# Kernel optimization log

Hardware: AMD Instinct MI355X
Metric: run time of the kernel (lower is better)

Reference implementation:

```python
import jax, jax.numpy as jnp
import numpy as np

VOCAB, EMBED, HIDDEN = 32000, 256, 512
N, L = 64, 2048

def setup_inputs() -> dict:
    key = jax.random.key(0)
    k1, k2, k3, k4 = jax.random.split(key, 4)
    X = jax.random.randint(k1, (N, L), 0, VOCAB)
    E = jax.random.normal(k2, (VOCAB, EMBED), dtype=jnp.float32) * 0.02
    W_hh = jax.random.normal(k3, (HIDDEN, HIDDEN), dtype=jnp.float32) / np.sqrt(HIDDEN)
    b_hh = jnp.zeros((HIDDEN,), dtype=jnp.float32)
    W_xh = jax.random.normal(k4, (EMBED, HIDDEN), dtype=jnp.float32) / np.sqrt(EMBED)
    b_xh = jnp.zeros((HIDDEN,), dtype=jnp.float32)
    return {"X": X, "E": E, "W_hh": W_hh, "b_hh": b_hh, "W_xh": W_xh, "b_xh": b_xh}

def reference(X, E, W_hh, b_hh, W_xh, b_xh):
    # Embed tokens: (N, L, De)
    xe = E[X]
    # Precompute input projection for all timesteps in one big GEMM: (N, L, H)
    xp = jnp.einsum('nld,dh->nlh', xe, W_xh) + b_xh
    h0 = jnp.zeros((X.shape[0], W_hh.shape[0]), dtype=E.dtype)

    def step(h, x_t):
        # h: (N, H); x_t: (N, H) already projected
        h_new = jnp.tanh(h @ W_hh + b_hh + x_t)
        return h_new, None

    # scan over time: move L to leading axis -> (L, N, H)
    h_last, _ = jax.lax.scan(step, h0, jnp.swapaxes(xp, 0, 1))
    return h_last
```

## Files before the change

kernel.cpp:

```cpp
#include <hip/hip_runtime.h>

typedef _Float16 h8 __attribute__((ext_vector_type(8)));
typedef float f4v __attribute__((ext_vector_type(4)));
typedef unsigned int u32;
typedef unsigned long long u64;
typedef u32 u32x4 __attribute__((ext_vector_type(4)));

#define SEQ 2048
#define HID 512
#define EMB 256
#define NV 32000
#define LOSCALE 2048.0f
#define INV_LOSCALE 4.8828125e-4f

#define WS_WHI 0u
#define WS_WLO (512u * 1024u)
#define WS_HG (1024u * 1024u)
#define WS_FLAGS (WS_HG + 256u * 1024u)
#define WS_PROJ (WS_FLAGS + 4u * 1024u)
#define FLAG_STRIDE 32

__global__ void wsplit_kernel(const float* __restrict__ Whh,
                              _Float16* __restrict__ Whi,
                              _Float16* __restrict__ Wlo) {
  int gid = blockIdx.x * 256 + threadIdx.x;
  int l = gid & 63, c = gid >> 6;
  int kb = c & 15, jtg = c >> 4;
  int j = jtg * 16 + (l & 15);
  int k0 = kb * 32 + (l >> 4) * 8;
  _Float16 hi[8], lo[8];
#pragma unroll
  for (int e = 0; e < 8; ++e) {
    float v = Whh[(k0 + e) * HID + j];
    _Float16 h = (_Float16)v;
    hi[e] = h;
    lo[e] = (_Float16)((v - (float)h) * LOSCALE);
  }
  *(h8*)(Whi + (size_t)gid * 8) = *(const h8*)hi;
  *(h8*)(Wlo + (size_t)gid * 8) = *(const h8*)lo;
}

template <bool PF32>
__global__ __launch_bounds__(256) void proj_kernel(const float* __restrict__ E,
                                                   const float* __restrict__ Wxh,
                                                   const float* __restrict__ bxh,
                                                   void* __restrict__ projE) {
  __shared__ float El[32 * EMB];
  const int t = threadIdx.x;
  const int v0 = blockIdx.x * 32;
  {
    const float4* src = (const float4*)(E + (size_t)v0 * EMB);
    float4* dst = (float4*)El;
#pragma unroll
    for (int i = 0; i < 8; ++i) dst[t + i * 256] = src[t + i * 256];
  }
  __syncthreads();
  const int c0 = (t & 63) * 8;
  const int rg = t >> 6;
  float acc[8][8];
#pragma unroll
  for (int r = 0; r < 8; ++r)
#pragma unroll
    for (int c = 0; c < 8; ++c) acc[r][c] = 0.f;

#pragma unroll 4
  for (int d = 0; d < EMB; ++d) {
    float wv[8];
    *(float4*)&wv[0] = *(const float4*)&Wxh[d * HID + c0];
    *(float4*)&wv[4] = *(const float4*)&Wxh[d * HID + c0 + 4];
#pragma unroll
    for (int r = 0; r < 8; ++r) {
      float ev = El[(rg * 8 + r) * EMB + d];
#pragma unroll
      for (int c = 0; c < 8; ++c) acc[r][c] = fmaf(ev, wv[c], acc[r][c]);
    }
  }
  float bv[8];
  *(float4*)&bv[0] = *(const float4*)&bxh[c0];
  *(float4*)&bv[4] = *(const float4*)&bxh[c0 + 4];
#pragma unroll
  for (int r = 0; r < 8; ++r) {
    int row = v0 + rg * 8 + r;
    if (PF32) {
      float o[8];
#pragma unroll
      for (int c = 0; c < 8; ++c) o[c] = acc[r][c] + bv[c];
      *(float4*)((float*)projE + (size_t)row * HID + c0) = *(const float4*)&o[0];
      *(float4*)((float*)projE + (size_t)row * HID + c0 + 4) = *(const float4*)&o[4];
    } else {
      _Float16 o[8];
#pragma unroll
      for (int c = 0; c < 8; ++c) o[c] = (_Float16)(acc[r][c] + bv[c]);
      *(h8*)((_Float16*)projE + (size_t)row * HID + c0) = *(const h8*)o;
    }
  }
}

__global__ void init_kernel(float4* __restrict__ p) {
  int gid = blockIdx.x * 256 + threadIdx.x;
  if (gid < 16640) p[gid] = (float4){0.f, 0.f, 0.f, 0.f};
}

template <bool PF32>
__global__ __launch_bounds__(512, 2) void rnn_kernel(
    const int* __restrict__ X, const _Float16* __restrict__ Whi,
    const _Float16* __restrict__ Wlo, const void* __restrict__ projE,
    const float* __restrict__ bhh, u32* __restrict__ hX,
    u32* __restrict__ flags, float* __restrict__ out) {
  __shared__ u32 hs[8192];
  const int tid = threadIdx.x;
  const int w = tid >> 6, lane = tid & 63;
  const int g = lane >> 4, li = lane & 15;
  const int grp = blockIdx.x >> 2, cb = blockIdx.x & 3;
  const int nb = grp * 16;
  const int jtg = cb * 8 + w;
  const int j = jtg * 16 + li;

  h8 Wh[16], Wl[16];
  {
    const char* wb = (const char*)Whi + ((size_t)jtg * 16 * 64 + lane) * 16;
    const char* wb2 = (const char*)Wlo + ((size_t)jtg * 16 * 64 + lane) * 16;
#pragma unroll
    for (int kb = 0; kb < 16; ++kb) {
      Wh[kb] = *(const h8*)(wb + (size_t)kb * 1024);
      Wl[kb] = *(const h8*)(wb2 + (size_t)kb * 1024);
    }
#pragma unroll
    for (int kb = 0; kb < 16; ++kb) {
      f4v th = __builtin_bit_cast(f4v, Wh[kb]);
      f4v tl = __builtin_bit_cast(f4v, Wl[kb]);
      asm volatile("" : "+v"(th), "+v"(tl));
      Wh[kb] = __builtin_bit_cast(h8, th);
      Wl[kb] = __builtin_bit_cast(h8, tl);
    }
  }
  const float bias = bhh[j];
  u32* fl = flags + grp * 4 * FLAG_STRIDE;

  const int hi2 = ((jtg & 1) << 1) | (li >> 3);
  const int pub0 = (li & 1) * 4096 + (jtg >> 1) * 256 + (hi2 << 6) + g * 16 +
                   ((li & 7) >> 1);
  u32* const hgrp = hX + grp * 8192;
  const bool oddli = (li & 1) != 0;

  const int* Xr[4];
#pragma unroll
  for (int i = 0; i < 4; ++i) Xr[i] = X + (size_t)(nb + g * 4 + i) * SEQ;

  for (int t = 0; t < SEQ; ++t) {
    float pv[4];
#pragma unroll
    for (int i = 0; i < 4; ++i) {
      int tok = Xr[i][t];
      if (PF32)
        pv[i] = ((const float*)projE)[(size_t)tok * HID + j];
      else
        pv[i] = (float)((const _Float16*)projE)[(size_t)tok * HID + j];
    }

    if (t > 0 && lane < 4) {
      u32 spins = 0;
      while (__hip_atomic_load(fl + lane * FLAG_STRIDE, __ATOMIC_RELAXED,
                               __HIP_MEMORY_SCOPE_AGENT) < (u32)t) {
        if (++spins > 10000u) break;
      }
    }

    {
      const u32* src = hgrp + (t & 1) * 32768;
      u64 v[4][2];
#pragma unroll
      for (int q = 0; q < 4; ++q) {
        int idx = tid * 4 + q * 2048;
        v[q][0] = __hip_atomic_load((const u64*)(src + idx), __ATOMIC_RELAXED,
                                    __HIP_MEMORY_SCOPE_AGENT);
        v[q][1] = __hip_atomic_load((const u64*)(src + idx + 2),
                                    __ATOMIC_RELAXED, __HIP_MEMORY_SCOPE_AGENT);
      }
#pragma unroll
      for (int q = 0; q < 4; ++q) {
        u32x4 d;
        d[0] = (u32)v[q][0]; d[1] = (u32)(v[q][0] >> 32);
        d[2] = (u32)v[q][1]; d[3] = (u32)(v[q][1] >> 32);
        *(u32x4*)(hs + tid * 4 + q * 2048) = d;
      }
    }
    __syncthreads();

    f4v a1 = {0.f, 0.f, 0.f, 0.f};
    f4v c1 = {0.f, 0.f, 0.f, 0.f};
    f4v c2 = {0.f, 0.f, 0.f, 0.f};
    const u32* hb_hi = hs + lane * 4;
    const u32* hb_lo = hs + 4096 + lane * 4;
#pragma unroll
    for (int kb = 0; kb < 16; ++kb) {
      h8 ahc = *(const h8*)(hb_hi + kb * 256);
      h8 alc = *(const h8*)(hb_lo + kb * 256);
      a1 = __builtin_amdgcn_mfma_f32_16x16x32_f16(ahc, Wh[kb], a1, 0, 0, 0);
      c1 = __builtin_amdgcn_mfma_f32_16x16x32_f16(ahc, Wl[kb], c1, 0, 0, 0);
      c2 = __builtin_amdgcn_mfma_f32_16x16x32_f16(alc, Wh[kb], c2, 0, 0, 0);
    }

    u32* const hn = hgrp + ((t + 1) & 1) * 32768;
    const bool lastt = (t == SEQ - 1);
#pragma unroll
    for (int i = 0; i < 4; ++i) {
      float v = a1[i] + INV_LOSCALE * (c1[i] + c2[i]) + bias + pv[i];
      float e2 = __expf(2.0f * v);
      float th = 1.0f - 2.0f / (e2 + 1.0f);
      _Float16 hh = (_Float16)th;
      _Float16 hl = (_Float16)((th - (float)hh) * LOSCALE);
      u32 pk = (u32)__builtin_bit_cast(unsigned short, hh) |
               ((u32)__builtin_bit_cast(unsigned short, hl) << 16);
      u32 nbv = (u32)__shfl_xor((int)pk, 1, 64);
      u32 word = oddli ? ((nbv >> 16) | (pk & 0xFFFF0000u))
                       : ((pk & 0xFFFFu) | (nbv << 16));
      __hip_atomic_store(hn + pub0 + i * 4, word, __ATOMIC_RELAXED,
                         __HIP_MEMORY_SCOPE_AGENT);
      if (lastt) out[(nb + g * 4 + i) * HID + j] = th;
    }
    __syncthreads();
    if (tid == 0) {
      __hip_atomic_store(fl + cb * FLAG_STRIDE, (u32)(t + 1), __ATOMIC_RELAXED,
                         __HIP_MEMORY_SCOPE_AGENT);
    }
  }
}

extern "C" void kernel_launch(void* const* d_in, const int* in_sizes, int n_in,
                              void* d_out, int out_size, void* d_ws,
                              size_t ws_size, hipStream_t stream) {
  const int* X = (const int*)d_in[0];
  const float* E = (const float*)d_in[1];
  const float* Whh = (const float*)d_in[2];
  const float* bhh = (const float*)d_in[3];
  const float* Wxh = (const float*)d_in[4];
  const float* bxh = (const float*)d_in[5];
  float* out = (float*)d_out;

  char* ws = (char*)d_ws;
  _Float16* Whi = (_Float16*)(ws + WS_WHI);
  _Float16* Wlo = (_Float16*)(ws + WS_WLO);
  u32* hX = (u32*)(ws + WS_HG);
  u32* flags = (u32*)(ws + WS_FLAGS);
  void* projE = (void*)(ws + WS_PROJ);
  const bool pf32 = ws_size >= (size_t)WS_PROJ + (size_t)NV * HID * sizeof(float);

  wsplit_kernel<<<128, 256, 0, stream>>>(Whh, Whi, Wlo);
  init_kernel<<<65, 256, 0, stream>>>((float4*)(ws + WS_HG));
  if (pf32) {
    proj_kernel<true><<<NV / 32, 256, 0, stream>>>(E, Wxh, bxh, projE);
    rnn_kernel<true><<<16, 512, 0, stream>>>(X, Whi, Wlo, projE, bhh, hX, flags, out);
  } else {
    proj_kernel<false><<<NV / 32, 256, 0, stream>>>(E, Wxh, bxh, projE);
    rnn_kernel<false><<<16, 512, 0, stream>>>(X, Whi, Wlo, projE, bhh, hX, flags, out);
  }
}
```

Measured before the change: 6.248 ms.

## Keep own hidden slice in double-buffered LDS and split flag waits per wave pair

Each block now writes its freshly computed hidden-state slice directly into a double-buffered shared array, so it only reloads the other three blocks' slices from global memory. Each wave pair waits on the flag of only the one peer block whose slice it loads, rather than every wave waiting on all four flags. This cuts global traffic and shortens the critical-path wait in the per-timestep cross-block exchange. It doubles LDS use and relies on correct ordering between the local writes and the barrier; the spin limit is also raised.

```diff
diff --git a/kernel.cpp b/kernel.cpp
--- a/kernel.cpp
+++ b/kernel.cpp
@@ -107,7 +107,7 @@
     const _Float16* __restrict__ Wlo, const void* __restrict__ projE,
     const float* __restrict__ bhh, u32* __restrict__ hX,
     u32* __restrict__ flags, float* __restrict__ out) {
-  __shared__ u32 hs[8192];
+  __shared__ u32 hs[2][8192];
   const int tid = threadIdx.x;
   const int w = tid >> 6, lane = tid & 63;
   const int g = lane >> 4, li = lane & 15;
@@ -115,6 +115,9 @@
   const int nb = grp * 16;
   const int jtg = cb * 8 + w;
   const int j = jtg * 16 + li;
+  const int pairq = w >> 1;
+  const bool ownpair = (pairq == cb);
+  const int p = (w & 1) * 64 + lane;
 
   h8 Wh[16], Wl[16];
   {
@@ -143,6 +146,9 @@
   u32* const hgrp = hX + grp * 8192;
   const bool oddli = (li & 1) != 0;
 
+#pragma unroll
+  for (int i = 0; i < 16; ++i) hs[0][tid + i * 512] = 0u;
+
   const int* Xr[4];
 #pragma unroll
   for (int i = 0; i < 4; ++i) Xr[i] = X + (size_t)(nb + g * 4 + i) * SEQ;
@@ -158,31 +164,36 @@
         pv[i] = (float)((const _Float16*)projE)[(size_t)tok * HID + j];
     }
 
-    if (t > 0 && lane < 4) {
-      u32 spins = 0;
-      while (__hip_atomic_load(fl + lane * FLAG_STRIDE, __ATOMIC_RELAXED,
-                               __HIP_MEMORY_SCOPE_AGENT) < (u32)t) {
-        if (++spins > 10000u) break;
+    if (!ownpair) {
+      if (t > 0 && lane == 0) {
+        u32 spins = 0;
+        while (__hip_atomic_load(fl + pairq * FLAG_STRIDE, __ATOMIC_RELAXED,
+                                 __HIP_MEMORY_SCOPE_AGENT) < (u32)t) {
+          if (++spins > 50000u) break;
+        }
       }
-    }
-
-    {
+      asm volatile("" ::: "memory");
       const u32* src = hgrp + (t & 1) * 32768;
-      u64 v[4][2];
-#pragma unroll
-      for (int q = 0; q < 4; ++q) {
-        int idx = tid * 4 + q * 2048;
-        v[q][0] = __hip_atomic_load((const u64*)(src + idx), __ATOMIC_RELAXED,
-                                    __HIP_MEMORY_SCOPE_AGENT);
-        v[q][1] = __hip_atomic_load((const u64*)(src + idx + 2),
-                                    __ATOMIC_RELAXED, __HIP_MEMORY_SCOPE_AGENT);
+      const int b0 = pairq * 1024 + p * 8;
+      u64 v[2][4];
+#pragma unroll
+      for (int c = 0; c < 2; ++c) {
+        const u32* s = src + b0 + c * 4096;
+#pragma unroll
+        for (int q = 0; q < 4; ++q)
+          v[c][q] = __hip_atomic_load((const u64*)(s + q * 2),
+                                      __ATOMIC_RELAXED,
+                                      __HIP_MEMORY_SCOPE_AGENT);
       }
 #pragma unroll
-      for (int q = 0; q < 4; ++q) {
-        u32x4 d;
-        d[0] = (u32)v[q][0]; d[1] = (u32)(v[q][0] >> 32);
-        d[2] = (u32)v[q][1]; d[3] = (u32)(v[q][1] >> 32);
-        *(u32x4*)(hs + tid * 4 + q * 2048) = d;
+      for (int c = 0; c < 2; ++c) {
+        u32x4 d0, d1;
+        d0[0] = (u32)v[c][0]; d0[1] = (u32)(v[c][0] >> 32);
+        d0[2] = (u32)v[c][1]; d0[3] = (u32)(v[c][1] >> 32);
+        d1[0] = (u32)v[c][2]; d1[1] = (u32)(v[c][2] >> 32);
+        d1[2] = (u32)v[c][3]; d1[3] = (u32)(v[c][3] >> 32);
+        *(u32x4*)(&hs[t & 1][b0 + c * 4096]) = d0;
+        *(u32x4*)(&hs[t & 1][b0 + c * 4096 + 4]) = d1;
       }
     }
     __syncthreads();
@@ -190,8 +201,8 @@
     f4v a1 = {0.f, 0.f, 0.f, 0.f};
     f4v c1 = {0.f, 0.f, 0.f, 0.f};
     f4v c2 = {0.f, 0.f, 0.f, 0.f};
-    const u32* hb_hi = hs + lane * 4;
-    const u32* hb_lo = hs + 4096 + lane * 4;
+    const u32* hb_hi = &hs[t & 1][lane * 4];
+    const u32* hb_lo = hb_hi + 4096;
 #pragma unroll
     for (int kb = 0; kb < 16; ++kb) {
       h8 ahc = *(const h8*)(hb_hi + kb * 256);
@@ -202,6 +213,7 @@
     }
 
     u32* const hn = hgrp + ((t + 1) & 1) * 32768;
+    u32* const hsn = hs[(t + 1) & 1];
     const bool lastt = (t == SEQ - 1);
 #pragma unroll
     for (int i = 0; i < 4; ++i) {
@@ -217,6 +229,7 @@
                        : ((pk & 0xFFFFu) | (nbv << 16));
       __hip_atomic_store(hn + pub0 + i * 4, word, __ATOMIC_RELAXED,
                          __HIP_MEMORY_SCOPE_AGENT);
+      hsn[pub0 + i * 4] = word;
       if (lastt) out[(nb + g * 4 + i) * HID + j] = th;
     }
     __syncthreads();
```

Measured after the change: 8.245 ms. +32.0%, slower.

## Replace flag-based inter-block sync with epoch bits embedded in published hidden state

Applied to the files above, without the earlier changes.

Drops the per-block progress flags and their spin-wait, and instead stores an epoch parity bit in the lowest mantissa bit of each published fp16 hi/lo half. Consumers keep reloading the hidden-state buffer until every word carries the expected epoch bit, then use the data directly. This removes the flag store, the flag poll round trip and the memory-ordering gap between them. In exchange it loses one mantissa bit of precision on some values, and whole-buffer polling may add memory traffic while waiting. The init kernel seeds the second buffer with epoch bit 1.

```diff
diff --git a/kernel.cpp b/kernel.cpp
--- a/kernel.cpp
+++ b/kernel.cpp
@@ -3,6 +3,7 @@
 typedef _Float16 h8 __attribute__((ext_vector_type(8)));
 typedef float f4v __attribute__((ext_vector_type(4)));
 typedef unsigned int u32;
+typedef unsigned short u16;
 typedef unsigned long long u64;
 typedef u32 u32x4 __attribute__((ext_vector_type(4)));
 
@@ -18,7 +19,6 @@
 #define WS_HG (1024u * 1024u)
 #define WS_FLAGS (WS_HG + 256u * 1024u)
 #define WS_PROJ (WS_FLAGS + 4u * 1024u)
-#define FLAG_STRIDE 32
 
 __global__ void wsplit_kernel(const float* __restrict__ Whh,
                               _Float16* __restrict__ Whi,
@@ -98,7 +98,14 @@
 
 __global__ void init_kernel(float4* __restrict__ p) {
   int gid = blockIdx.x * 256 + threadIdx.x;
-  if (gid < 16640) p[gid] = (float4){0.f, 0.f, 0.f, 0.f};
+  if (gid < 16640) {
+    float4 z = {0.f, 0.f, 0.f, 0.f};
+    if (gid >= 8192 && gid < 16384) {
+      float one = __uint_as_float(1u);
+      z = (float4){one, one, one, one};
+    }
+    p[gid] = z;
+  }
 }
 
 template <bool PF32>
@@ -106,7 +113,7 @@
     const int* __restrict__ X, const _Float16* __restrict__ Whi,
     const _Float16* __restrict__ Wlo, const void* __restrict__ projE,
     const float* __restrict__ bhh, u32* __restrict__ hX,
-    u32* __restrict__ flags, float* __restrict__ out) {
+    float* __restrict__ out) {
   __shared__ u32 hs[8192];
   const int tid = threadIdx.x;
   const int w = tid >> 6, lane = tid & 63;
@@ -135,7 +142,6 @@
     }
   }
   const float bias = bhh[j];
-  u32* fl = flags + grp * 4 * FLAG_STRIDE;
 
   const int hi2 = ((jtg & 1) << 1) | (li >> 3);
   const int pub0 = (li & 1) * 4096 + (jtg >> 1) * 256 + (hi2 << 6) + g * 16 +
@@ -158,32 +164,39 @@
         pv[i] = (float)((const _Float16*)projE)[(size_t)tok * HID + j];
     }
 
-    if (t > 0 && lane < 4) {
-      u32 spins = 0;
-      while (__hip_atomic_load(fl + lane * FLAG_STRIDE, __ATOMIC_RELAXED,
-                               __HIP_MEMORY_SCOPE_AGENT) < (u32)t) {
-        if (++spins > 10000u) break;
+    const u32 e = (u32)(t >> 1) & 1u;
+    const u32* src = hgrp + (t & 1) * 32768 + tid * 4;
+    u64 v[4][2];
+    {
+      int tries = 0;
+      while (true) {
+#pragma unroll
+        for (int q = 0; q < 4; ++q) {
+          v[q][0] = __hip_atomic_load((const u64*)(src + q * 2048),
+                                      __ATOMIC_RELAXED,
+                                      __HIP_MEMORY_SCOPE_AGENT);
+          v[q][1] = __hip_atomic_load((const u64*)(src + q * 2048 + 2),
+                                      __ATOMIC_RELAXED,
+                                      __HIP_MEMORY_SCOPE_AGENT);
+        }
+        u64 orr = (v[0][0] | v[0][1]) | (v[1][0] | v[1][1]) |
+                  (v[2][0] | v[2][1]) | (v[3][0] | v[3][1]);
+        u64 andd = (v[0][0] & v[0][1]) & (v[1][0] & v[1][1]) &
+                   (v[2][0] & v[2][1]) & (v[3][0] & v[3][1]);
+        bool ok;
+        if (e)
+          ok = ((andd & 1ull) != 0) && (((andd >> 32) & 1ull) != 0);
+        else
+          ok = ((orr & 1ull) == 0) && (((orr >> 32) & 1ull) == 0);
+        if (__all(ok) || ++tries > 200000) break;
       }
     }
-
-    {
-      const u32* src = hgrp + (t & 1) * 32768;
-      u64 v[4][2];
-#pragma unroll
-      for (int q = 0; q < 4; ++q) {
-        int idx = tid * 4 + q * 2048;
-        v[q][0] = __hip_atomic_load((const u64*)(src + idx), __ATOMIC_RELAXED,
-                                    __HIP_MEMORY_SCOPE_AGENT);
-        v[q][1] = __hip_atomic_load((const u64*)(src + idx + 2),
-                                    __ATOMIC_RELAXED, __HIP_MEMORY_SCOPE_AGENT);
-      }
-#pragma unroll
-      for (int q = 0; q < 4; ++q) {
-        u32x4 d;
-        d[0] = (u32)v[q][0]; d[1] = (u32)(v[q][0] >> 32);
-        d[2] = (u32)v[q][1]; d[3] = (u32)(v[q][1] >> 32);
-        *(u32x4*)(hs + tid * 4 + q * 2048) = d;
-      }
+#pragma unroll
+    for (int q = 0; q < 4; ++q) {
+      u32x4 d;
+      d[0] = (u32)v[q][0]; d[1] = (u32)(v[q][0] >> 32);
+      d[2] = (u32)v[q][1]; d[3] = (u32)(v[q][1] >> 32);
+      *(u32x4*)(hs + tid * 4 + q * 2048) = d;
     }
     __syncthreads();
 
@@ -191,7 +204,7 @@
     f4v c1 = {0.f, 0.f, 0.f, 0.f};
     f4v c2 = {0.f, 0.f, 0.f, 0.f};
     const u32* hb_hi = hs + lane * 4;
-    const u32* hb_lo = hs + 4096 + lane * 4;
+    const u32* hb_lo = hb_hi + 4096;
 #pragma unroll
     for (int kb = 0; kb < 16; ++kb) {
       h8 ahc = *(const h8*)(hb_hi + kb * 256);
@@ -202,16 +215,21 @@
     }
 
     u32* const hn = hgrp + ((t + 1) & 1) * 32768;
+    const u32 ep = (u32)((t + 1) >> 1) & 1u;
     const bool lastt = (t == SEQ - 1);
 #pragma unroll
     for (int i = 0; i < 4; ++i) {
-      float v = a1[i] + INV_LOSCALE * (c1[i] + c2[i]) + bias + pv[i];
-      float e2 = __expf(2.0f * v);
+      float vfull = a1[i] + INV_LOSCALE * (c1[i] + c2[i]) + bias + pv[i];
+      float e2 = __expf(2.0f * vfull);
       float th = 1.0f - 2.0f / (e2 + 1.0f);
       _Float16 hh = (_Float16)th;
+      u16 h16 = __builtin_bit_cast(u16, hh);
+      if (!oddli) h16 = (u16)((h16 & 0xFFFEu) | ep);
+      hh = __builtin_bit_cast(_Float16, h16);
       _Float16 hl = (_Float16)((th - (float)hh) * LOSCALE);
-      u32 pk = (u32)__builtin_bit_cast(unsigned short, hh) |
-               ((u32)__builtin_bit_cast(unsigned short, hl) << 16);
+      u16 l16 = __builtin_bit_cast(u16, hl);
+      if (!oddli) l16 = (u16)((l16 & 0xFFFEu) | ep);
+      u32 pk = (u32)h16 | ((u32)l16 << 16);
       u32 nbv = (u32)__shfl_xor((int)pk, 1, 64);
       u32 word = oddli ? ((nbv >> 16) | (pk & 0xFFFF0000u))
                        : ((pk & 0xFFFFu) | (nbv << 16));
@@ -220,10 +238,6 @@
       if (lastt) out[(nb + g * 4 + i) * HID + j] = th;
     }
     __syncthreads();
-    if (tid == 0) {
-      __hip_atomic_store(fl + cb * FLAG_STRIDE, (u32)(t + 1), __ATOMIC_RELAXED,
-                         __HIP_MEMORY_SCOPE_AGENT);
-    }
   }
 }
 
@@ -242,7 +256,6 @@
   _Float16* Whi = (_Float16*)(ws + WS_WHI);
   _Float16* Wlo = (_Float16*)(ws + WS_WLO);
   u32* hX = (u32*)(ws + WS_HG);
-  u32* flags = (u32*)(ws + WS_FLAGS);
   void* projE = (void*)(ws + WS_PROJ);
   const bool pf32 = ws_size >= (size_t)WS_PROJ + (size_t)NV * HID * sizeof(float);
 
@@ -250,9 +263,9 @@
   init_kernel<<<65, 256, 0, stream>>>((float4*)(ws + WS_HG));
   if (pf32) {
     proj_kernel<true><<<NV / 32, 256, 0, stream>>>(E, Wxh, bxh, projE);
-    rnn_kernel<true><<<16, 512, 0, stream>>>(X, Whi, Wlo, projE, bhh, hX, flags, out);
+    rnn_kernel<true><<<16, 512, 0, stream>>>(X, Whi, Wlo, projE, bhh, hX, out);
   } else {
     proj_kernel<false><<<NV / 32, 256, 0, stream>>>(E, Wxh, bxh, projE);
-    rnn_kernel<false><<<16, 512, 0, stream>>>(X, Whi, Wlo, projE, bhh, hX, flags, out);
-  }
-}
+    rnn_kernel<false><<<16, 512, 0, stream>>>(X, Whi, Wlo, projE, bhh, hX, out);
+  }
+}
```

After: 6.453 ms. 1.03x slower.
